# Kernel tuning notes

Hardware: AMD Instinct MI355X
Metric: run time of the kernel (lower is better)

The kernel has to match this reference:

```python
import jax, jax.numpy as jnp
import numpy as np

DIM = 2048
N_EXPERTS = 8
TOP_K = 2


def setup_inputs() -> dict:
    key = jax.random.key(0)
    ks = jax.random.split(key, 5)
    x = jax.random.normal(ks[0], (4, 4096, DIM), dtype=jnp.float32)
    # Linear(dim, dim, bias=False) stores weight as [out, in]; y = x @ W.T
    W_up = jax.random.normal(ks[1], (DIM, DIM), dtype=jnp.float32) * (1.0 / np.sqrt(DIM))
    W_down = jax.random.normal(ks[2], (DIM, DIM), dtype=jnp.float32) * (1.0 / np.sqrt(DIM))
    W_gate = jax.random.normal(ks[3], (N_EXPERTS, DIM), dtype=jnp.float32) * (1.0 / np.sqrt(DIM))
    # expert_weight: nn.Parameter(torch.randn(dim, dim)), applied as x @ W_expert
    W_expert = jax.random.normal(ks[4], (DIM, DIM), dtype=jnp.float32) * (1.0 / np.sqrt(DIM))
    return {"x": x, "W_up": W_up, "W_down": W_down, "W_gate": W_gate, "W_expert": W_expert}


def reference(x, W_up, W_down, W_gate, W_expert):
    # Gating: logits [B,S,E], top-k routing
    logits = jnp.einsum("bsd,ed->bse", x, W_gate)
    routing_weights, selected_experts = jax.lax.top_k(logits, TOP_K)  # [B,S,K]
    # Shared expert MLP
    shared_out = jnp.einsum("bsd,od->bso", jax.nn.relu(jnp.einsum("bsd,od->bso", x, W_up)), W_down)
    # Mock MoE combine: all selected experts share a single weight matrix, so the
    # dispatch-compute-scatter collapses to a softmax-normalized weighted sum of the
    # same expert output per token (weights sum to 1 over k).
    rw = jax.nn.softmax(routing_weights, axis=-1)  # [B,S,K]
    expert_out = jnp.einsum("bsd,do->bso", x, W_expert)  # shared across selected experts
    moe_out = jnp.sum(rw, axis=-1, keepdims=True) * expert_out
    return shared_out + moe_out
```

## Files before the change

kernel.cpp:

```cpp
#include <hip/hip_runtime.h>
#include <hip/hip_bf16.h>
#include <stdint.h>


#define DIM 2048
#define MTOT 16384

typedef unsigned short u16;
typedef __bf16 bf16x8 __attribute__((ext_vector_type(8)));
typedef float f32x4 __attribute__((ext_vector_type(4)));

__device__ __forceinline__ u16 f2bf(float f) {
    union { float f; unsigned int u; } a; a.f = f;
    unsigned int u = a.u;
    unsigned int r = (u + 0x7fffu + ((u >> 16) & 1u)) >> 16;
    return (u16)r;
}

__device__ __forceinline__ bf16x8 frag_load(const void* p) {
    union { uint4 u; bf16x8 b; } x;
    x.u = *(const uint4*)p;
    return x.b;
}

__global__ void cvt_all(const float* __restrict__ x, const float* __restrict__ Wu,
                        const float* __restrict__ Wd, u16* __restrict__ Abig,
                        u16* __restrict__ Wup, u16* __restrict__ Bbig) {
    const long NX = (long)MTOT * DIM / 4;
    const long NW = (long)DIM * DIM / 4;
    long i = (long)blockIdx.x * blockDim.x + threadIdx.x;
    long stride = (long)gridDim.x * blockDim.x;
    for (; i < NX + 2 * NW; i += stride) {
        const float* src; u16* dst; int dld, doff; long e;
        if (i < NX)            { src = x;  dst = Abig; dld = 4096; doff = 2048; e = i << 2; }
        else if (i < NX + NW)  { src = Wu; dst = Wup;  dld = 2048; doff = 0;    e = (i - NX) << 2; }
        else                   { src = Wd; dst = Bbig; dld = 4096; doff = 0;    e = (i - NX - NW) << 2; }
        long row = e >> 11;
        int col = (int)(e & 2047);
        float4 v = *(const float4*)(src + e);
        union { u16 q[4]; uint2 d; } u;
        u.q[0] = f2bf(v.x); u.q[1] = f2bf(v.y);
        u.q[2] = f2bf(v.z); u.q[3] = f2bf(v.w);
        *(uint2*)(dst + row * (long)dld + doff + col) = u.d;
    }
}

__global__ void cvt_transpose(const float* __restrict__ W, u16* __restrict__ dst) {
    __shared__ float t[32][33];
    int bx = blockIdx.x & 63;
    int by = blockIdx.x >> 6;
    int x = threadIdx.x & 31, y = threadIdx.x >> 5;
    #pragma unroll
    for (int j = 0; j < 32; j += 8)
        t[y + j][x] = W[(size_t)(by * 32 + y + j) * 2048 + bx * 32 + x];
    __syncthreads();
    #pragma unroll
    for (int j = 0; j < 32; j += 8)
        dst[(size_t)(bx * 32 + y + j) * 4096 + 2048 + by * 32 + x] = f2bf(t[x][y + j]);
}

template <int MODE>
__global__ __launch_bounds__(512, 2)
void gemm256(const u16* __restrict__ A, const u16* __restrict__ B,
             void* __restrict__ Cptr, int lda, int ldb, int K) {
    __shared__ char lds[2][65536];

    const int tid  = threadIdx.x;
    const int lane = tid & 63;
    const int wv   = tid >> 6;
    const int wr   = wv >> 2;
    const int wc   = wv & 3;

    int bid = blockIdx.x;
    int cpx = gridDim.x >> 3;
    int swz = (bid & 7) * cpx + (bid >> 3);
    int tile_n = swz & 7;
    int tile_m = swz >> 3;

    const int rowA0 = tile_m * 256;
    const int rowB0 = tile_n * 256;

    const int r_sub = tid >> 3;
    const int c_src = ((tid & 7) ^ (r_sub & 7)) << 3;
    const u16* pAb = A + (size_t)(rowA0 + r_sub) * lda + c_src;
    const u16* pBb = B + (size_t)(rowB0 + r_sub) * ldb + c_src;

    f32x4 acc[2][2][4][2];
    #pragma unroll
    for (int a = 0; a < 2; ++a)
        #pragma unroll
        for (int b = 0; b < 2; ++b)
            #pragma unroll
            for (int m = 0; m < 4; ++m)
                #pragma unroll
                for (int n = 0; n < 2; ++n)
                    acc[a][b][m][n] = (f32x4){0.f, 0.f, 0.f, 0.f};

    bf16x8 av[4][2];
    bf16x8 bva[2][2];
    bf16x8 bvb[2][2];
    const int kA = (lane >> 4) << 4;

#define STAGE_A(H, KOFF, BUF) do {                                              \
    const u16* _s = pAb + (size_t)((H) * 128) * lda + (KOFF);                   \
    __builtin_amdgcn_global_load_lds(                                           \
        (const __attribute__((address_space(1))) void*)_s,                      \
        (__attribute__((address_space(3))) void*)((char*)lds[BUF] + (H)*16384 + (wv<<10)), \
        16, 0, 0);                                                              \
    __builtin_amdgcn_global_load_lds(                                           \
        (const __attribute__((address_space(1))) void*)(_s + (size_t)64 * lda), \
        (__attribute__((address_space(3))) void*)((char*)lds[BUF] + (H)*16384 + 8192 + (wv<<10)), \
        16, 0, 0);                                                              \
  } while (0)

#define STAGE_B(H, KOFF, BUF) do {                                              \
    const u16* _s = pBb + (size_t)((H) * 128) * ldb + (KOFF);                   \
    __builtin_amdgcn_global_load_lds(                                           \
        (const __attribute__((address_space(1))) void*)_s,                      \
        (__attribute__((address_space(3))) void*)((char*)lds[BUF] + 32768 + (H)*16384 + (wv<<10)), \
        16, 0, 0);                                                              \
    __builtin_amdgcn_global_load_lds(                                           \
        (const __attribute__((address_space(1))) void*)(_s + (size_t)64 * ldb), \
        (__attribute__((address_space(3))) void*)((char*)lds[BUF] + 32768 + (H)*16384 + 8192 + (wv<<10)), \
        16, 0, 0);                                                              \
  } while (0)

#define DSREAD_A(MH, CUR) do {                                                  \
    _Pragma("unroll")                                                           \
    for (int m = 0; m < 4; ++m) {                                               \
        int ra = (wr << 6) + (m << 4) + (lane & 15);                            \
        const char* _b = (const char*)lds[CUR] + (MH)*16384 + (ra << 7);        \
        int sw = (ra & 7) << 4;                                                 \
        av[m][0] = frag_load(_b + (kA ^ sw));                                   \
        av[m][1] = frag_load(_b + ((64 + kA) ^ sw));                            \
    } } while (0)

#define DSREAD_B(NH, CUR, DST) do {                                             \
    _Pragma("unroll")                                                           \
    for (int n = 0; n < 2; ++n) {                                               \
        int rb = (wc << 5) + (n << 4) + (lane & 15);                            \
        const char* _b = (const char*)lds[CUR] + 32768 + (NH)*16384 + (rb << 7);\
        int sw = (rb & 7) << 4;                                                 \
        DST[n][0] = frag_load(_b + (kA ^ sw));                                  \
        DST[n][1] = frag_load(_b + ((64 + kA) ^ sw));                           \
    } } while (0)

#define MFMA_Q(MH, NH, BV) do {                                                 \
    __builtin_amdgcn_s_setprio(1);                                              \
    _Pragma("unroll")                                                           \
    for (int m = 0; m < 4; ++m)                                                 \
        _Pragma("unroll")                                                       \
        for (int n = 0; n < 2; ++n) {                                           \
            acc[MH][NH][m][n] = __builtin_amdgcn_mfma_f32_16x16x32_bf16(        \
                av[m][0], BV[n][0], acc[MH][NH][m][n], 0, 0, 0);                \
            acc[MH][NH][m][n] = __builtin_amdgcn_mfma_f32_16x16x32_bf16(        \
                av[m][1], BV[n][1], acc[MH][NH][m][n], 0, 0, 0);                \
        }                                                                       \
    __builtin_amdgcn_s_setprio(0);                                              \
  } while (0)

#define WAIT_VM(N) asm volatile("s_waitcnt vmcnt(" #N ")" ::: "memory")
#define BAR() __builtin_amdgcn_s_barrier()

    STAGE_A(0, 0, 0);
    STAGE_B(0, 0, 0);
    STAGE_B(1, 0, 0);
    STAGE_A(1, 0, 0);
    WAIT_VM(4);
    BAR();

    const int nK = K >> 6;
    int cur = 0;
    for (int t = 0; t < nK - 1; ++t) {
        const int koff = (t + 1) << 6;
        const int nxt = cur ^ 1;
        DSREAD_A(0, cur);
        DSREAD_B(0, cur, bva);
        STAGE_A(0, koff, nxt);
        STAGE_B(0, koff, nxt);
        WAIT_VM(6); BAR();
        MFMA_Q(0, 0, bva);
        DSREAD_B(1, cur, bvb);
        STAGE_B(1, koff, nxt);
        WAIT_VM(6); BAR();
        MFMA_Q(0, 1, bvb);
        DSREAD_A(1, cur);
        STAGE_A(1, koff, nxt);
        BAR();
        MFMA_Q(1, 1, bvb);
        WAIT_VM(4); BAR();
        MFMA_Q(1, 0, bva);
        cur = nxt;
    }

    DSREAD_A(0, cur);
    DSREAD_B(0, cur, bva);
    WAIT_VM(2); BAR();
    MFMA_Q(0, 0, bva);
    DSREAD_B(1, cur, bvb);
    WAIT_VM(0); BAR();
    MFMA_Q(0, 1, bvb);
    DSREAD_A(1, cur);
    MFMA_Q(1, 1, bvb);
    MFMA_Q(1, 0, bva);

    #pragma unroll
    for (int mh = 0; mh < 2; ++mh)
        #pragma unroll
        for (int m = 0; m < 4; ++m)
            #pragma unroll
            for (int r = 0; r < 4; ++r) {
                int row = rowA0 + mh * 128 + (wr << 6) + (m << 4) + ((lane >> 4) << 2) + r;
                #pragma unroll
                for (int nh = 0; nh < 2; ++nh)
                    #pragma unroll
                    for (int n = 0; n < 2; ++n) {
                        int col = tile_n * 256 + nh * 128 + (wc << 5) + (n << 4) + (lane & 15);
                        float v = acc[mh][nh][m][n][r];
                        if (MODE == 0) {
                            ((u16*)Cptr)[(size_t)row * 4096 + col] = f2bf(fmaxf(v, 0.f));
                        } else {
                            ((float*)Cptr)[(size_t)row * 2048 + col] = v;
                        }
                    }
            }
#undef STAGE_A
#undef STAGE_B
#undef DSREAD_A
#undef DSREAD_B
#undef MFMA_Q
#undef WAIT_VM
#undef BAR
}

extern "C" void kernel_launch(void* const* d_in, const int* in_sizes, int n_in,
                              void* d_out, int out_size, void* d_ws, size_t ws_size,
                              hipStream_t stream) {
    const float* x        = (const float*)d_in[0];
    const float* W_up     = (const float*)d_in[1];
    const float* W_down   = (const float*)d_in[2];
    const float* W_expert = (const float*)d_in[4];

    u16* Abig = (u16*)d_ws;
    u16* Bbig = Abig + (size_t)MTOT * 4096;
    u16* Wup  = Bbig + (size_t)DIM * 4096;

    cvt_all<<<2048, 256, 0, stream>>>(x, W_up, W_down, Abig, Wup, Bbig);
    cvt_transpose<<<4096, 256, 0, stream>>>(W_expert, Bbig);

    gemm256<0><<<512, 512, 0, stream>>>(Abig + 2048, Wup, Abig, 4096, 2048, 2048);
    gemm256<1><<<512, 512, 0, stream>>>(Abig, Bbig, d_out, 4096, 4096, 4096);
}
```

Measured before the change: 389.3 us.

## Load B fragments directly from global into registers, bypassing LDS

The B operand is no longer staged through LDS. Each wave loads its B MFMA fragments straight from global memory into registers, prefetched one K-step ahead, while A keeps the LDS double buffer. LDS use is halved and two barriers per iteration go away. In exchange, B global loads are replicated across the two wave rows and are less coalesced (16-byte pieces from separate rows), and register pressure rises, which could hurt under the 2-blocks-per-CU launch bound.

```diff
diff --git a/kernel.cpp b/kernel.cpp
--- a/kernel.cpp
+++ b/kernel.cpp
@@ -63,7 +63,7 @@
 __global__ __launch_bounds__(512, 2)
 void gemm256(const u16* __restrict__ A, const u16* __restrict__ B,
              void* __restrict__ Cptr, int lda, int ldb, int K) {
-    __shared__ char lds[2][65536];
+    __shared__ char lds[2][32768];
 
     const int tid  = threadIdx.x;
     const int lane = tid & 63;
@@ -83,7 +83,9 @@
     const int r_sub = tid >> 3;
     const int c_src = ((tid & 7) ^ (r_sub & 7)) << 3;
     const u16* pAb = A + (size_t)(rowA0 + r_sub) * lda + c_src;
-    const u16* pBb = B + (size_t)(rowB0 + r_sub) * ldb + c_src;
+
+    const u16* pBf = B + (size_t)(rowB0 + (wc << 5) + (lane & 15)) * ldb
+                       + ((lane >> 4) << 3);
 
     f32x4 acc[2][2][4][2];
     #pragma unroll
@@ -113,18 +115,6 @@
         16, 0, 0);                                                              \
   } while (0)
 
-#define STAGE_B(H, KOFF, BUF) do {                                              \
-    const u16* _s = pBb + (size_t)((H) * 128) * ldb + (KOFF);                   \
-    __builtin_amdgcn_global_load_lds(                                           \
-        (const __attribute__((address_space(1))) void*)_s,                      \
-        (__attribute__((address_space(3))) void*)((char*)lds[BUF] + 32768 + (H)*16384 + (wv<<10)), \
-        16, 0, 0);                                                              \
-    __builtin_amdgcn_global_load_lds(                                           \
-        (const __attribute__((address_space(1))) void*)(_s + (size_t)64 * ldb), \
-        (__attribute__((address_space(3))) void*)((char*)lds[BUF] + 32768 + (H)*16384 + 8192 + (wv<<10)), \
-        16, 0, 0);                                                              \
-  } while (0)
-
 #define DSREAD_A(MH, CUR) do {                                                  \
     _Pragma("unroll")                                                           \
     for (int m = 0; m < 4; ++m) {                                               \
@@ -135,15 +125,21 @@
         av[m][1] = frag_load(_b + ((64 + kA) ^ sw));                            \
     } } while (0)
 
-#define DSREAD_B(NH, CUR, DST) do {                                             \
-    _Pragma("unroll")                                                           \
-    for (int n = 0; n < 2; ++n) {                                               \
-        int rb = (wc << 5) + (n << 4) + (lane & 15);                            \
-        const char* _b = (const char*)lds[CUR] + 32768 + (NH)*16384 + (rb << 7);\
-        int sw = (rb & 7) << 4;                                                 \
-        DST[n][0] = frag_load(_b + (kA ^ sw));                                  \
-        DST[n][1] = frag_load(_b + ((64 + kA) ^ sw));                           \
-    } } while (0)
+#define LOAD_BVA(KOFFE) do {                                                    \
+    const u16* _p = pBf + (KOFFE);                                              \
+    bva[0][0] = frag_load(_p);                                                  \
+    bva[0][1] = frag_load(_p + 32);                                             \
+    bva[1][0] = frag_load(_p + (size_t)16 * ldb);                               \
+    bva[1][1] = frag_load(_p + (size_t)16 * ldb + 32);                          \
+  } while (0)
+
+#define LOAD_BVB(KOFFE) do {                                                    \
+    const u16* _p = pBf + (size_t)128 * ldb + (KOFFE);                          \
+    bvb[0][0] = frag_load(_p);                                                  \
+    bvb[0][1] = frag_load(_p + 32);                                             \
+    bvb[1][0] = frag_load(_p + (size_t)16 * ldb);                               \
+    bvb[1][1] = frag_load(_p + (size_t)16 * ldb + 32);                          \
+  } while (0)
 
 #define MFMA_Q(MH, NH, BV) do {                                                 \
     __builtin_amdgcn_s_setprio(1);                                              \
@@ -160,13 +156,15 @@
   } while (0)
 
 #define WAIT_VM(N) asm volatile("s_waitcnt vmcnt(" #N ")" ::: "memory")
+#define FENCE() asm volatile("" ::: "memory")
 #define BAR() __builtin_amdgcn_s_barrier()
 
     STAGE_A(0, 0, 0);
-    STAGE_B(0, 0, 0);
-    STAGE_B(1, 0, 0);
     STAGE_A(1, 0, 0);
-    WAIT_VM(4);
+    FENCE();
+    LOAD_BVA(0);
+    LOAD_BVB(0);
+    WAIT_VM(8);
     BAR();
 
     const int nK = K >> 6;
@@ -175,30 +173,23 @@
         const int koff = (t + 1) << 6;
         const int nxt = cur ^ 1;
         DSREAD_A(0, cur);
-        DSREAD_B(0, cur, bva);
         STAGE_A(0, koff, nxt);
-        STAGE_B(0, koff, nxt);
-        WAIT_VM(6); BAR();
+        STAGE_A(1, koff, nxt);
+        FENCE();
         MFMA_Q(0, 0, bva);
-        DSREAD_B(1, cur, bvb);
-        STAGE_B(1, koff, nxt);
-        WAIT_VM(6); BAR();
         MFMA_Q(0, 1, bvb);
         DSREAD_A(1, cur);
-        STAGE_A(1, koff, nxt);
+        MFMA_Q(1, 1, bvb);
+        LOAD_BVB(koff);
+        MFMA_Q(1, 0, bva);
+        LOAD_BVA(koff);
+        WAIT_VM(8);
         BAR();
-        MFMA_Q(1, 1, bvb);
-        WAIT_VM(4); BAR();
-        MFMA_Q(1, 0, bva);
         cur = nxt;
     }
 
     DSREAD_A(0, cur);
-    DSREAD_B(0, cur, bva);
-    WAIT_VM(2); BAR();
     MFMA_Q(0, 0, bva);
-    DSREAD_B(1, cur, bvb);
-    WAIT_VM(0); BAR();
     MFMA_Q(0, 1, bvb);
     DSREAD_A(1, cur);
     MFMA_Q(1, 1, bvb);
@@ -225,11 +216,12 @@
                     }
             }
 #undef STAGE_A
-#undef STAGE_B
 #undef DSREAD_A
-#undef DSREAD_B
+#undef LOAD_BVA
+#undef LOAD_BVB
 #undef MFMA_Q
 #undef WAIT_VM
+#undef FENCE
 #undef BAR
 }
 
```

Result: slower. 507.7 us (+30.4%).
